# Performance work log

Hardware: AMD Instinct MI355X
Metric: run time of the kernel (lower is better)

## Reference

```python
import jax, jax.numpy as jnp
import numpy as np
import math

NC = 80
TOPK = 10
EPS = 1e-9
DIS = 2.5
BIG = 1e5


def _ciou(b1, b2, eps=EPS):
    # b1: (bs,1,A,4), b2: (bs,G,1,4) -> (bs,G,A)
    b1x1, b1y1, b1x2, b1y2 = b1[..., 0], b1[..., 1], b1[..., 2], b1[..., 3]
    b2x1, b2y1, b2x2, b2y2 = b2[..., 0], b2[..., 1], b2[..., 2], b2[..., 3]
    w1, h1 = b1x2 - b1x1, b1y2 - b1y1 + eps
    w2, h2 = b2x2 - b2x1, b2y2 - b2y1 + eps
    iw = jnp.clip(jnp.minimum(b1x2, b2x2) - jnp.maximum(b1x1, b2x1), 0.0)
    ih = jnp.clip(jnp.minimum(b1y2, b2y2) - jnp.maximum(b1y1, b2y1), 0.0)
    inter = iw * ih
    union = w1 * h1 + w2 * h2 - inter + eps
    iou = inter / union
    cw = jnp.maximum(b1x2, b2x2) - jnp.minimum(b1x1, b2x1)
    ch = jnp.maximum(b1y2, b2y2) - jnp.minimum(b1y1, b2y1)
    c2 = cw * cw + ch * ch + eps
    d2 = ((b2x1 + b2x2 - b1x1 - b1x2) ** 2 + (b2y1 + b2y2 - b1y1 - b1y2) ** 2) / 4.0
    v = (4.0 / math.pi ** 2) * (jnp.arctan(w2 / h2) - jnp.arctan(w1 / h1)) ** 2
    alpha = jax.lax.stop_gradient(v / (v - iou + (1.0 + eps)))
    return iou - (d2 / c2 + v * alpha)


def _cost_matrix(pred_boxes, gt_boxes, mask_gt, pred_scores, gt_labels):
    # geometric candidate masks
    pc = (pred_boxes[..., :2] + pred_boxes[..., 2:]) / 2.0  # (bs,A,2) anchor centers
    pce = pc[:, None, :, :]                                  # (bs,1,A,2)
    in_boxes = jnp.all(pce > gt_boxes[:, :, None, :2], -1) & jnp.all(gt_boxes[:, :, None, 2:] > pce, -1)
    gcen = (gt_boxes[..., :2] + gt_boxes[..., 2:]) / 2.0
    in_centers = jnp.all(pce > (gcen - DIS)[:, :, None, :], -1) & jnp.all((gcen + DIS)[:, :, None, :] > pce, -1)
    both = in_boxes & in_centers                             # (bs,G,A)

    ciou_val = _ciou(pred_boxes[:, None, :, :], gt_boxes[:, :, None, :])  # (bs,G,A)

    # summed BCE over classes against one-hot(gt_label), without (bs,G,A,nc) intermediate:
    # sum_c bce = -sum_c log(1-p_c) - (log p_y - log(1-p_y))
    p = jnp.clip(pred_scores, 1e-7, 1.0 - 1e-7)
    logp = jnp.log(p)
    log1mp = jnp.log1p(-p)
    S = -log1mp.sum(-1)                                      # (bs,A)
    delta = -(logp - log1mp)                                 # (bs,A,nc)
    per_lab = jnp.take_along_axis(jnp.transpose(delta, (0, 2, 1)), gt_labels[:, :, None], axis=1)  # (bs,G,A)
    cls_cost = S[:, None, :] + per_lab

    cost = cls_cost + 3.0 * ciou_val + BIG * (~both).astype(cost_dtype(pred_boxes))
    return cost


def cost_dtype(x):
    return x.dtype


def reference(pred_boxes, gt_boxes, mask_gt, pred_scores, gt_labels):
    cost = _cost_matrix(pred_boxes, gt_boxes, mask_gt, pred_scores, gt_labels)  # (bs,G,A)
    bs, G, A = cost.shape
    # per-GT bottom-k (lowest cost) candidate anchors
    _, idx = jax.lax.top_k(-cost, TOPK)                      # (bs,G,TOPK)
    b_ix = jnp.arange(bs)[:, None, None]
    g_ix = jnp.arange(G)[None, :, None]
    pt_mask = jnp.zeros((bs, G, A), dtype=bool).at[b_ix, g_ix, idx].set(True)
    pt_mask = pt_mask & mask_gt[:, :, None]
    # conflict resolution: anchors claimed by >1 GT go to the min-cost GT
    overlap = pt_mask.sum(1) > 1                             # (bs,A)
    pick = jnp.argmin(jnp.where(pt_mask, cost, jnp.inf), axis=1)  # (bs,A)
    pick_oh = jnp.arange(G)[None, :, None] == pick[:, None, :]    # (bs,G,A)
    final = jnp.where(overlap[:, None, :], pick_oh, pt_mask) & mask_gt[:, :, None]
    return final, cost


def setup_inputs() -> dict:
    key = jax.random.key(0)
    k = jax.random.split(key, 7)
    bs, A, G = 32, 8400, 64
    pc = jax.random.uniform(k[0], (bs, A, 2)) * 640.0
    pwh = jax.random.uniform(k[1], (bs, A, 2)) * 96.0 + 8.0
    pred_boxes = jnp.concatenate([pc - pwh / 2, pc + pwh / 2], -1)
    gc = jax.random.uniform(k[2], (bs, G, 2)) * 640.0
    gwh = jax.random.uniform(k[3], (bs, G, 2)) * 128.0 + 16.0
    gt_boxes = jnp.concatenate([gc - gwh / 2, gc + gwh / 2], -1)
    mask_gt = jax.random.uniform(k[4], (bs, G)) < 0.8
    pred_scores = jax.random.uniform(k[5], (bs, A, NC), minval=1e-4, maxval=1.0 - 1e-4)
    gt_labels = jax.random.randint(k[6], (bs, G), 0, NC, dtype=jnp.int32)
    return {"pred_boxes": pred_boxes, "gt_boxes": gt_boxes, "mask_gt": mask_gt,
            "pred_scores": pred_scores, "gt_labels": gt_labels}
```

## Files before the change

### kernel.cpp

```cpp
#include <hip/hip_runtime.h>
#include <math.h>

#define BS   32
#define A_N  8400
#define G_N  64
#define NC_N 80
#define TK   10

static __device__ __forceinline__ float fdiv(float n, float d) {
    return n * __builtin_amdgcn_rcpf(d);
}
static __device__ __forceinline__ unsigned sortable(float f) {
    unsigned u = __float_as_uint(f);
    return (u & 0x80000000u) ? ~u : (u | 0x80000000u);
}

__global__ __launch_bounds__(256)
void k_cost(const float* __restrict__ pred_boxes,
            const float* __restrict__ gt_boxes,
            const float* __restrict__ pred_scores,
            const int*   __restrict__ gt_labels,
            float* __restrict__ cost)
{
    __shared__ float s_gx1[G_N], s_gy1[G_N], s_gx2[G_N], s_gy2[G_N];
    __shared__ float s_gsx[G_N], s_gsy[G_N];
    __shared__ float s_glx[G_N], s_gly[G_N], s_ghx[G_N], s_ghy[G_N];
    __shared__ float s_area2[G_N], s_atg[G_N];
    __shared__ int   s_lab[G_N];
    __shared__ int   s_ord[G_N];
    __shared__ int   s_seg0[NC_N], s_seg1[NC_N];

    const float EPSF = 1e-9f;
    const int t = threadIdx.x;
    const int b = blockIdx.y;
    const int a = blockIdx.x * 256 + t;

    if (t < G_N) {
        const float4 gb = ((const float4*)gt_boxes)[b * G_N + t];
        const float gx1 = gb.x, gy1 = gb.y, gx2 = gb.z, gy2 = gb.w;
        s_gx1[t] = gx1; s_gy1[t] = gy1; s_gx2[t] = gx2; s_gy2[t] = gy2;
        const float sx = gx1 + gx2, sy = gy1 + gy2;
        s_gsx[t] = sx; s_gsy[t] = sy;
        const float cx = sx / 2.0f, cy = sy / 2.0f;
        s_glx[t] = cx - 2.5f; s_ghx[t] = cx + 2.5f;
        s_gly[t] = cy - 2.5f; s_ghy[t] = cy + 2.5f;
        const float w2 = gx2 - gx1;
        const float h2 = (gy2 - gy1) + EPSF;
        s_area2[t] = w2 * h2;
        s_atg[t]   = atanf(w2 / h2);
        s_lab[t]   = gt_labels[b * G_N + t];
    }
    __syncthreads();
    if (t < G_N) {
        const int myl = s_lab[t];
        int rank = 0;
        for (int j = 0; j < G_N; ++j) {
            const int lj = s_lab[j];
            rank += (lj < myl) || (lj == myl && j < t);
        }
        s_ord[rank] = t;
    }
    if (t < NC_N) {
        int lo = 0, hi = 0;
        for (int j = 0; j < G_N; ++j) {
            lo += (s_lab[j] <  t);
            hi += (s_lab[j] <= t);
        }
        s_seg0[t] = lo; s_seg1[t] = hi;
    }
    __syncthreads();
    if (a >= A_N) return;

    const float* prow = pred_scores + ((size_t)b * A_N + a) * NC_N;
    const float4* p4 = (const float4*)prow;
    const float LO = 1e-7f;
    const float HI = (float)(1.0 - 1e-7);

    float prod = 1.0f, Sacc = 0.0f;
    for (int c4 = 0; c4 < NC_N / 4; ++c4) {
        const float4 pv = p4[c4];
        const float ps[4] = {pv.x, pv.y, pv.z, pv.w};
        #pragma unroll
        for (int j = 0; j < 4; ++j) {
            const float pc = fminf(fmaxf(ps[j], LO), HI);
            prod *= (1.0f - pc);
        }
        if (c4 & 1) { Sacc += logf(prod); prod = 1.0f; }
    }
    const float S = -Sacc;

    const float4 pb = ((const float4*)pred_boxes)[(size_t)b * A_N + a];
    const float pcx  = (pb.x + pb.z) / 2.0f;
    const float pcy  = (pb.y + pb.w) / 2.0f;
    const float w1   = pb.z - pb.x;
    const float h1   = (pb.w - pb.y) + EPSF;
    const float area1 = w1 * h1;
    const float atp  = atanf(w1 / h1);
    const float KPI  = (float)(4.0 / (M_PI * M_PI));

    float* crow = cost + (size_t)b * G_N * A_N + a;

    for (int c4 = NC_N / 4 - 1; c4 >= 0; --c4) {
        if (s_seg1[c4 * 4 + 3] <= s_seg0[c4 * 4]) continue;
        const float4 pv = p4[c4];
        const float ps[4] = {pv.x, pv.y, pv.z, pv.w};
        #pragma unroll
        for (int j = 3; j >= 0; --j) {
            const int c  = c4 * 4 + j;
            const int lo = s_seg0[c], hi = s_seg1[c];
            if (lo >= hi) continue;
            const float pc = fminf(fmaxf(ps[j], LO), HI);
            const float Sd = S + logf((1.0f - pc) * __builtin_amdgcn_rcpf(pc));
            for (int k = lo; k < hi; ++k) {
                const int g = s_ord[k];
                const float gx1 = s_gx1[g], gy1 = s_gy1[g];
                const float gx2 = s_gx2[g], gy2 = s_gy2[g];
                const bool inb  = (pcx > gx1) && (pcy > gy1) && (gx2 > pcx) && (gy2 > pcy);
                const bool inc  = (pcx > s_glx[g]) && (pcy > s_gly[g]) &&
                                  (s_ghx[g] > pcx) && (s_ghy[g] > pcy);
                const bool both = inb && inc;

                const float iw    = fmaxf(fminf(pb.z, gx2) - fmaxf(pb.x, gx1), 0.0f);
                const float ih    = fmaxf(fminf(pb.w, gy2) - fmaxf(pb.y, gy1), 0.0f);
                const float inter = iw * ih;
                const float uni   = ((area1 + s_area2[g]) - inter) + EPSF;
                const float iou   = fdiv(inter, uni);
                const float cw    = fmaxf(pb.z, gx2) - fminf(pb.x, gx1);
                const float ch    = fmaxf(pb.w, gy2) - fminf(pb.y, gy1);
                const float c2    = ((cw * cw) + (ch * ch)) + EPSF;
                const float dx    = (s_gsx[g] - pb.x) - pb.z;
                const float dy    = (s_gsy[g] - pb.y) - pb.w;
                const float d2    = ((dx * dx) + (dy * dy)) / 4.0f;
                const float dif   = s_atg[g] - atp;
                const float v     = KPI * (dif * dif);
                const float alpha = fdiv(v, (v - iou) + 1.0f);
                const float ciou  = iou - (fdiv(d2, c2) + v * alpha);

                const float cst   = (Sd + 3.0f * ciou) + (both ? 0.0f : 100000.0f);
                crow[(size_t)g * A_N] = cst;
            }
        }
    }
}

__global__ __launch_bounds__(256)
void k_topk(const float* __restrict__ cost, int* __restrict__ topk)
{
    __shared__ unsigned long long s_w[4][TK];

    const int bg   = blockIdx.x;
    const int t    = threadIdx.x;
    const int lane = t & 63;
    const int wid  = t >> 6;
    const float* row = cost + (size_t)bg * A_N;
    const unsigned long long UMAX = ~0ull;

    unsigned long long v[TK];
    #pragma unroll
    for (int j = 0; j < TK; ++j) v[j] = UMAX;

    auto consider = [&](float c, int idx) {
        const unsigned long long key =
            ((unsigned long long)sortable(c) << 14) | (unsigned)idx;
        if (key < v[TK - 1]) {
            v[TK - 1] = key;
            #pragma unroll
            for (int j = TK - 2; j >= 0; --j) {
                const bool sw = v[j + 1] < v[j];
                const unsigned long long tv = v[j];
                v[j]     = sw ? v[j + 1] : v[j];
                v[j + 1] = sw ? tv : v[j + 1];
            }
        }
    };

    const float4* row4 = (const float4*)row;
    const int NV = A_N / 4;
    float4 cur = make_float4(0.f, 0.f, 0.f, 0.f);
    if (t < NV) cur = row4[t];
    for (int i = t; i < NV; i += 256) {
        const int i2 = i + 256;
        float4 nxt = make_float4(0.f, 0.f, 0.f, 0.f);
        if (i2 < NV) nxt = row4[i2];
        const int base = i * 4;
        consider(cur.x, base);
        consider(cur.y, base + 1);
        consider(cur.z, base + 2);
        consider(cur.w, base + 3);
        cur = nxt;
    }

    #pragma unroll
    for (int r = 0; r < TK; ++r) {
        unsigned long long bv = v[0];
        #pragma unroll
        for (int off = 1; off < 64; off <<= 1) {
            const unsigned long long ov = __shfl_xor(bv, off, 64);
            bv = (ov < bv) ? ov : bv;
        }
        if (lane == 0) s_w[wid][r] = bv;
        if (v[0] == bv) {
            #pragma unroll
            for (int j = 0; j < TK - 1; ++j) v[j] = v[j + 1];
            v[TK - 1] = UMAX;
        }
    }
    __syncthreads();

    if (wid == 0) {
        unsigned long long cv = UMAX;
        if (lane < 4 * TK) cv = s_w[lane / TK][lane % TK];
        #pragma unroll
        for (int r = 0; r < TK; ++r) {
            unsigned long long bv = cv;
            #pragma unroll
            for (int off = 1; off < 64; off <<= 1) {
                const unsigned long long ov = __shfl_xor(bv, off, 64);
                bv = (ov < bv) ? ov : bv;
            }
            if (lane == 0) topk[bg * TK + r] = (int)(bv & 16383ull);
            if (cv == bv) cv = UMAX;
        }
    }
}

__global__ __launch_bounds__(256)
void k_scatter1(const float* __restrict__ cost,
                const int*   __restrict__ topk,
                const unsigned char* __restrict__ mask_gt,
                unsigned long long* __restrict__ slot)
{
    const int e = blockIdx.x * 256 + threadIdx.x;
    if (e >= BS * G_N * TK) return;
    const int b = e / (G_N * TK);
    const int r = e % (G_N * TK);
    const int g = r / TK;
    if (!mask_gt[b * G_N + g]) return;
    const int a = topk[e];
    const float c = cost[((size_t)b * G_N + g) * A_N + a];
    const unsigned long long key = ((unsigned long long)sortable(c) << 6) | (unsigned)g;
    atomicMin(&slot[(size_t)b * A_N + a], key);
}

__global__ __launch_bounds__(256)
void k_scatter2(const int* __restrict__ topk,
                const unsigned char* __restrict__ mask_gt,
                const unsigned long long* __restrict__ slot,
                float* __restrict__ final_out)
{
    const int e = blockIdx.x * 256 + threadIdx.x;
    if (e >= BS * G_N * TK) return;
    const int b = e / (G_N * TK);
    const int r = e % (G_N * TK);
    const int g = r / TK;
    if (!mask_gt[b * G_N + g]) return;
    const int a = topk[e];
    if ((int)(slot[(size_t)b * A_N + a] & 63ull) == g)
        final_out[((size_t)b * G_N + g) * A_N + a] = 1.0f;
}

__global__ __launch_bounds__(256)
void k_final(const float* __restrict__ cost,
             const int*   __restrict__ topk,
             const unsigned char* __restrict__ mask_gt,
             float* __restrict__ final_out)
{
    __shared__ int s_top[G_N * TK];
    __shared__ int s_mask[G_N];

    const int t = threadIdx.x;
    const int b = blockIdx.y;
    const int a = blockIdx.x * 256 + t;

    for (int k = t; k < G_N * TK; k += 256) s_top[k] = topk[b * G_N * TK + k];
    if (t < G_N) s_mask[t] = (int)mask_gt[b * G_N + t];
    __syncthreads();
    if (a >= A_N) return;

    unsigned long long member = 0ull;
    int cnt = 0;
    float best = __builtin_inff();
    int bestg = 0;
    for (int g = 0; g < G_N; ++g) {
        bool m = false;
        if (s_mask[g]) {
            #pragma unroll
            for (int j = 0; j < TK; ++j) m = m || (s_top[g * TK + j] == a);
        }
        if (m) {
            member |= (1ull << g);
            ++cnt;
            const float c = cost[((size_t)b * G_N + g) * A_N + a];
            if (c < best) { best = c; bestg = g; }
        }
    }
    const bool ovl = cnt > 1;
    float* frow = final_out + (size_t)b * G_N * A_N + a;
    for (int g = 0; g < G_N; ++g) {
        const bool f = ovl ? (g == bestg) : (((member >> g) & 1ull) != 0ull);
        frow[(size_t)g * A_N] = f ? 1.0f : 0.0f;
    }
}

extern "C" void kernel_launch(void* const* d_in, const int* in_sizes, int n_in,
                              void* d_out, int out_size, void* d_ws, size_t ws_size,
                              hipStream_t stream)
{
    const float* pred_boxes  = (const float*)d_in[0];
    const float* gt_boxes    = (const float*)d_in[1];
    const unsigned char* mask_gt = (const unsigned char*)d_in[2];
    const float* pred_scores = (const float*)d_in[3];
    const int*   gt_labels   = (const int*)d_in[4];

    float* out_final = (float*)d_out;
    float* out_cost  = out_final + (size_t)BS * G_N * A_N;

    const size_t slot_bytes = (size_t)BS * A_N * sizeof(unsigned long long);
    const size_t topk_bytes = (size_t)BS * G_N * TK * sizeof(int);
    unsigned long long* slot = (unsigned long long*)d_ws;
    int* topk_ws = (int*)((char*)d_ws + slot_bytes);
    const bool sparse_ok = ws_size >= slot_bytes + topk_bytes;
    if (!sparse_ok) topk_ws = (int*)d_ws;

    k_cost <<<dim3((A_N + 255) / 256, BS), 256, 0, stream>>>(
        pred_boxes, gt_boxes, pred_scores, gt_labels, out_cost);
    k_topk <<<dim3(BS * G_N), 256, 0, stream>>>(out_cost, topk_ws);

    if (sparse_ok) {
        hipMemsetAsync(out_final, 0, (size_t)BS * G_N * A_N * sizeof(float), stream);
        hipMemsetAsync(slot, 0xFF, slot_bytes, stream);
        const int NE = BS * G_N * TK;
        k_scatter1<<<dim3((NE + 255) / 256), 256, 0, stream>>>(
            out_cost, topk_ws, mask_gt, slot);
        k_scatter2<<<dim3((NE + 255) / 256), 256, 0, stream>>>(
            topk_ws, mask_gt, slot, out_final);
    } else {
        k_final<<<dim3((A_N + 255) / 256, BS), 256, 0, stream>>>(
            out_cost, topk_ws, mask_gt, out_final);
    }
}
```

Baseline: 334.7 us.

## Preload scores once, stage per-label deltas in LDS, fuse memsets into one init kernel

The cost kernel now loads all 80 class scores per anchor into registers once and precomputes the per-label log-ratio deltas into a shared-memory table, filling it in two halves of 32 distinct labels. It then emits costs in label-sorted GT order, reading box data as packed float4 from LDS. The two hipMemsetAsync calls are replaced by one grid-stride init kernel launched before the cost kernel. The aim is fewer redundant global score reads, fewer divergent per-class branches and less launch overhead, in exchange for high register pressure (80 floats per thread) and 32 KB of LDS per block, both of which may reduce occupancy.

New measurement: 379.1 us. 13.3% more time.

```diff
diff --git a/kernel.cpp b/kernel.cpp
--- a/kernel.cpp
+++ b/kernel.cpp
@@ -6,6 +6,7 @@
 #define G_N  64
 #define NC_N 80
 #define TK   10
+#define HALF_R 32
 
 static __device__ __forceinline__ float fdiv(float n, float d) {
     return n * __builtin_amdgcn_rcpf(d);
@@ -22,13 +23,13 @@
             const int*   __restrict__ gt_labels,
             float* __restrict__ cost)
 {
-    __shared__ float s_gx1[G_N], s_gy1[G_N], s_gx2[G_N], s_gy2[G_N];
-    __shared__ float s_gsx[G_N], s_gsy[G_N];
-    __shared__ float s_glx[G_N], s_gly[G_N], s_ghx[G_N], s_ghy[G_N];
-    __shared__ float s_area2[G_N], s_atg[G_N];
-    __shared__ int   s_lab[G_N];
-    __shared__ int   s_ord[G_N];
-    __shared__ int   s_seg0[NC_N], s_seg1[NC_N];
+    __shared__ float4 s_box[G_N];
+    __shared__ float4 s_mid[G_N];
+    __shared__ float4 s_ctr[G_N];
+    __shared__ int    s_lab[G_N], s_ord[G_N], s_rowk[G_N];
+    __shared__ int    s_pres[NC_N], s_rank[NC_N];
+    __shared__ int    s_split;
+    __shared__ float  s_delta[HALF_R * 256];
 
     const float EPSF = 1e-9f;
     const int t = threadIdx.x;
@@ -37,18 +38,13 @@
 
     if (t < G_N) {
         const float4 gb = ((const float4*)gt_boxes)[b * G_N + t];
-        const float gx1 = gb.x, gy1 = gb.y, gx2 = gb.z, gy2 = gb.w;
-        s_gx1[t] = gx1; s_gy1[t] = gy1; s_gx2[t] = gx2; s_gy2[t] = gy2;
-        const float sx = gx1 + gx2, sy = gy1 + gy2;
-        s_gsx[t] = sx; s_gsy[t] = sy;
+        s_box[t] = gb;
+        const float sx = gb.x + gb.z, sy = gb.y + gb.w;
+        const float w2 = gb.z - gb.x, h2 = (gb.w - gb.y) + EPSF;
+        s_mid[t] = make_float4(sx, sy, w2 * h2, atanf(w2 / h2));
         const float cx = sx / 2.0f, cy = sy / 2.0f;
-        s_glx[t] = cx - 2.5f; s_ghx[t] = cx + 2.5f;
-        s_gly[t] = cy - 2.5f; s_ghy[t] = cy + 2.5f;
-        const float w2 = gx2 - gx1;
-        const float h2 = (gy2 - gy1) + EPSF;
-        s_area2[t] = w2 * h2;
-        s_atg[t]   = atanf(w2 / h2);
-        s_lab[t]   = gt_labels[b * G_N + t];
+        s_ctr[t] = make_float4(cx - 2.5f, cy - 2.5f, cx + 2.5f, cy + 2.5f);
+        s_lab[t] = gt_labels[b * G_N + t];
     }
     __syncthreads();
     if (t < G_N) {
@@ -61,31 +57,46 @@
         s_ord[rank] = t;
     }
     if (t < NC_N) {
-        int lo = 0, hi = 0;
-        for (int j = 0; j < G_N; ++j) {
-            lo += (s_lab[j] <  t);
-            hi += (s_lab[j] <= t);
-        }
-        s_seg0[t] = lo; s_seg1[t] = hi;
+        int p = 0;
+        for (int j = 0; j < G_N; ++j) p |= (s_lab[j] == t);
+        s_pres[t] = p;
+    }
+    __syncthreads();
+    if (t < NC_N) {
+        int r = 0;
+        for (int c = 0; c < t; ++c) r += s_pres[c];
+        s_rank[t] = s_pres[t] ? r : -1;
+    }
+    __syncthreads();
+    if (t < G_N)
+        s_rowk[t] = s_rank[s_lab[s_ord[t]]];
+    __syncthreads();
+    if (t == 0) {
+        int sp = G_N;
+        for (int k = 0; k < G_N; ++k)
+            if (s_rowk[k] >= HALF_R) { sp = k; break; }
+        s_split = sp;
     }
     __syncthreads();
     if (a >= A_N) return;
 
-    const float* prow = pred_scores + ((size_t)b * A_N + a) * NC_N;
-    const float4* p4 = (const float4*)prow;
+    const float4* p4 = (const float4*)(pred_scores + ((size_t)b * A_N + a) * NC_N);
+    float4 sc[20];
+    #pragma unroll
+    for (int i = 0; i < 20; ++i) sc[i] = p4[i];
+
     const float LO = 1e-7f;
     const float HI = (float)(1.0 - 1e-7);
-
     float prod = 1.0f, Sacc = 0.0f;
-    for (int c4 = 0; c4 < NC_N / 4; ++c4) {
-        const float4 pv = p4[c4];
-        const float ps[4] = {pv.x, pv.y, pv.z, pv.w};
-        #pragma unroll
-        for (int j = 0; j < 4; ++j) {
-            const float pc = fminf(fmaxf(ps[j], LO), HI);
-            prod *= (1.0f - pc);
-        }
-        if (c4 & 1) { Sacc += logf(prod); prod = 1.0f; }
+    #pragma unroll
+    for (int i = 0; i < 20; ++i) {
+        sc[i].x = fminf(fmaxf(sc[i].x, LO), HI);
+        sc[i].y = fminf(fmaxf(sc[i].y, LO), HI);
+        sc[i].z = fminf(fmaxf(sc[i].z, LO), HI);
+        sc[i].w = fminf(fmaxf(sc[i].w, LO), HI);
+        prod *= (1.0f - sc[i].x); prod *= (1.0f - sc[i].y);
+        prod *= (1.0f - sc[i].z); prod *= (1.0f - sc[i].w);
+        if (i & 1) { Sacc += logf(prod); prod = 1.0f; }
     }
     const float S = -Sacc;
 
@@ -97,50 +108,74 @@
     const float area1 = w1 * h1;
     const float atp  = atanf(w1 / h1);
     const float KPI  = (float)(4.0 / (M_PI * M_PI));
-
     float* crow = cost + (size_t)b * G_N * A_N + a;
-
-    for (int c4 = NC_N / 4 - 1; c4 >= 0; --c4) {
-        if (s_seg1[c4 * 4 + 3] <= s_seg0[c4 * 4]) continue;
-        const float4 pv = p4[c4];
-        const float ps[4] = {pv.x, pv.y, pv.z, pv.w};
+    const int split = s_split;
+
+    auto fillDelta = [&](int rlo) {
         #pragma unroll
-        for (int j = 3; j >= 0; --j) {
-            const int c  = c4 * 4 + j;
-            const int lo = s_seg0[c], hi = s_seg1[c];
-            if (lo >= hi) continue;
-            const float pc = fminf(fmaxf(ps[j], LO), HI);
-            const float Sd = S + logf((1.0f - pc) * __builtin_amdgcn_rcpf(pc));
-            for (int k = lo; k < hi; ++k) {
-                const int g = s_ord[k];
-                const float gx1 = s_gx1[g], gy1 = s_gy1[g];
-                const float gx2 = s_gx2[g], gy2 = s_gy2[g];
-                const bool inb  = (pcx > gx1) && (pcy > gy1) && (gx2 > pcx) && (gy2 > pcy);
-                const bool inc  = (pcx > s_glx[g]) && (pcy > s_gly[g]) &&
-                                  (s_ghx[g] > pcx) && (s_ghy[g] > pcy);
-                const bool both = inb && inc;
-
-                const float iw    = fmaxf(fminf(pb.z, gx2) - fmaxf(pb.x, gx1), 0.0f);
-                const float ih    = fmaxf(fminf(pb.w, gy2) - fmaxf(pb.y, gy1), 0.0f);
-                const float inter = iw * ih;
-                const float uni   = ((area1 + s_area2[g]) - inter) + EPSF;
-                const float iou   = fdiv(inter, uni);
-                const float cw    = fmaxf(pb.z, gx2) - fminf(pb.x, gx1);
-                const float ch    = fmaxf(pb.w, gy2) - fminf(pb.y, gy1);
-                const float c2    = ((cw * cw) + (ch * ch)) + EPSF;
-                const float dx    = (s_gsx[g] - pb.x) - pb.z;
-                const float dy    = (s_gsy[g] - pb.y) - pb.w;
-                const float d2    = ((dx * dx) + (dy * dy)) / 4.0f;
-                const float dif   = s_atg[g] - atp;
-                const float v     = KPI * (dif * dif);
-                const float alpha = fdiv(v, (v - iou) + 1.0f);
-                const float ciou  = iou - (fdiv(d2, c2) + v * alpha);
-
-                const float cst   = (Sd + 3.0f * ciou) + (both ? 0.0f : 100000.0f);
-                crow[(size_t)g * A_N] = cst;
+        for (int i = 0; i < 20; ++i) {
+            const float pv[4] = {sc[i].x, sc[i].y, sc[i].z, sc[i].w};
+            #pragma unroll
+            for (int j = 0; j < 4; ++j) {
+                const int r = s_rank[i * 4 + j];
+                if (r >= rlo && r < rlo + HALF_R)
+                    s_delta[(r - rlo) * 256 + t] =
+                        logf((1.0f - pv[j]) * __builtin_amdgcn_rcpf(pv[j]));
             }
         }
-    }
+    };
+    auto emitRange = [&](int k0, int k1, int rbase) {
+        for (int k = k0; k < k1; ++k) {
+            const int g = s_ord[k];
+            const float delta = s_delta[(s_rowk[k] - rbase) * 256 + t];
+            const float Sd = S + delta;
+            const float4 gb = s_box[g];
+            const float4 gm = s_mid[g];
+            const float4 gc = s_ctr[g];
+            const bool inb  = (pcx > gb.x) && (pcy > gb.y) && (gb.z > pcx) && (gb.w > pcy);
+            const bool inc  = (pcx > gc.x) && (pcy > gc.y) && (gc.z > pcx) && (gc.w > pcy);
+            const bool both = inb && inc;
+
+            const float iw    = fmaxf(fminf(pb.z, gb.z) - fmaxf(pb.x, gb.x), 0.0f);
+            const float ih    = fmaxf(fminf(pb.w, gb.w) - fmaxf(pb.y, gb.y), 0.0f);
+            const float inter = iw * ih;
+            const float uni   = ((area1 + gm.z) - inter) + EPSF;
+            const float iou   = fdiv(inter, uni);
+            const float cw    = fmaxf(pb.z, gb.z) - fminf(pb.x, gb.x);
+            const float ch    = fmaxf(pb.w, gb.w) - fminf(pb.y, gb.y);
+            const float c2    = ((cw * cw) + (ch * ch)) + EPSF;
+            const float dx    = (gm.x - pb.x) - pb.z;
+            const float dy    = (gm.y - pb.y) - pb.w;
+            const float d2    = ((dx * dx) + (dy * dy)) / 4.0f;
+            const float dif   = gm.w - atp;
+            const float v     = KPI * (dif * dif);
+            const float alpha = fdiv(v, (v - iou) + 1.0f);
+            const float ciou  = iou - (fdiv(d2, c2) + v * alpha);
+
+            const float cst   = (Sd + 3.0f * ciou) + (both ? 0.0f : 100000.0f);
+            crow[(size_t)g * A_N] = cst;
+        }
+    };
+
+    fillDelta(0);
+    emitRange(0, split, 0);
+    if (split < G_N) {
+        fillDelta(HALF_R);
+        emitRange(split, G_N, HALF_R);
+    }
+}
+
+__global__ __launch_bounds__(256)
+void k_init(float4* __restrict__ fin, long nf4,
+            uint4* __restrict__ slt, long ns4)
+{
+    const long stride = (long)gridDim.x * 256;
+    const float4 z4 = make_float4(0.f, 0.f, 0.f, 0.f);
+    const uint4  m4 = make_uint4(~0u, ~0u, ~0u, ~0u);
+    for (long i = (long)blockIdx.x * 256 + threadIdx.x; i < nf4; i += stride)
+        fin[i] = z4;
+    for (long i = (long)blockIdx.x * 256 + threadIdx.x; i < ns4; i += stride)
+        slt[i] = m4;
 }
 
 __global__ __launch_bounds__(256)
@@ -322,13 +357,18 @@
     const bool sparse_ok = ws_size >= slot_bytes + topk_bytes;
     if (!sparse_ok) topk_ws = (int*)d_ws;
 
+    if (sparse_ok) {
+        const long nf4 = (long)BS * G_N * A_N / 4;
+        const long ns4 = (long)BS * A_N / 2;
+        k_init<<<dim3(2048), 256, 0, stream>>>((float4*)out_final, nf4,
+                                               (uint4*)slot, ns4);
+    }
+
     k_cost <<<dim3((A_N + 255) / 256, BS), 256, 0, stream>>>(
         pred_boxes, gt_boxes, pred_scores, gt_labels, out_cost);
     k_topk <<<dim3(BS * G_N), 256, 0, stream>>>(out_cost, topk_ws);
 
     if (sparse_ok) {
-        hipMemsetAsync(out_final, 0, (size_t)BS * G_N * A_N * sizeof(float), stream);
-        hipMemsetAsync(slot, 0xFF, slot_bytes, stream);
         const int NE = BS * G_N * TK;
         k_scatter1<<<dim3((NE + 255) / 256), 256, 0, stream>>>(
             out_cost, topk_ws, mask_gt, slot);
```
